# Performance work log

Hardware: AMD Instinct MI355X
Metric: run time of the kernel (lower is better)

## Reference

```python
import jax, jax.numpy as jnp
import numpy as np

BINS = 73
VMIN = -10.0
VMAX = 10.0
EPS = 1e-5


def _bn_conv(x, g, b):
    # x: [B, C, N], batch-norm (training mode) over (batch, spatial)
    m = x.mean(axis=(0, 2), keepdims=True)
    v = x.var(axis=(0, 2), keepdims=True)
    return (x - m) * jax.lax.rsqrt(v + EPS) * g[None, :, None] + b[None, :, None]


def _bn_fc(x, g, b):
    # x: [B, C]
    m = x.mean(axis=0, keepdims=True)
    v = x.var(axis=0, keepdims=True)
    return (x - m) * jax.lax.rsqrt(v + EPS) * g[None, :] + b[None, :]


def _batch_hist(x):
    # Faithful port of the torch offset-trick histc + argmax pooling.
    # x: [B, F, N] -> [B, F] float (argmax bin index per (batch, feature))
    B, F, N = x.shape
    span = VMAX - VMIN  # 20.0
    # linspace(0, span*F*B, F*B+1)[:-1] has step exactly span
    offsets = span * jnp.arange(B * F, dtype=x.dtype)  # [B*F]
    xf = x.reshape(B * F, N) + offsets[:, None]
    total_bins = BINS * B * F
    total_max = span * B * F + VMIN
    width = (total_max - VMIN) / total_bins  # == span / BINS
    flat = xf.reshape(-1)
    idx = jnp.floor((flat - VMIN) / width).astype(jnp.int32)
    # torch.histc ignores out-of-range values; values == max fall in last bin
    in_range = (flat >= VMIN) & (flat <= total_max)
    idx = jnp.clip(idx, 0, total_bins - 1)
    counts = jnp.zeros(total_bins, dtype=x.dtype).at[idx].add(
        in_range.astype(x.dtype))
    hist = counts.reshape(B, F, BINS)
    # torch.max returns first max index, as does jnp.argmax
    return jnp.argmax(hist, axis=2).astype(x.dtype)  # [B, F]


def _forward(x, w1, b1, g1, be1, w2, b2, g2, be2, w3, b3, g3, be3,
             fw1, fb1, g4, be4, fw2, fb2, g5, be5, fw3, fb3):
    B = x.shape[0]
    # pointwise conv (k=1) == channel matmul
    h = jax.nn.relu(_bn_conv(jnp.einsum('oc,bcn->bon', w1, x) + b1[None, :, None], g1, be1))
    h = jax.nn.relu(_bn_conv(jnp.einsum('oc,bcn->bon', w2, h) + b2[None, :, None], g2, be2))
    h = jax.nn.relu(_bn_conv(jnp.einsum('oc,bcn->bon', w3, h) + b3[None, :, None], g3, be3))
    feat = jax.lax.stop_gradient(_batch_hist(h))  # [B, 1024]; hist/argmax is non-differentiable in torch too
    h = jax.nn.relu(_bn_fc(feat @ fw1.T + fb1, g4, be4))
    h = jax.nn.relu(_bn_fc(h @ fw2.T + fb2, g5, be5))
    out = h @ fw3.T + fb3  # [B, 9]
    iden = jnp.eye(3, dtype=x.dtype).reshape(1, 9)
    return (out + iden).reshape(-1, 3, 3)


def setup_inputs() -> dict:
    key = jax.random.key(0)
    ks = jax.random.split(key, 12)
    B, N = 16, 2048

    def w(k, shape):
        fan_in = shape[-1]
        return (jax.random.normal(k, shape) / np.sqrt(fan_in)).astype(jnp.float32)

    f32 = jnp.float32
    return {
        'x': jax.random.normal(ks[0], (B, 3, N), dtype=f32),
        'w1': w(ks[1], (64, 3)), 'b1': jnp.zeros(64, f32),
        'g1': jnp.ones(64, f32), 'be1': jnp.zeros(64, f32),
        'w2': w(ks[2], (128, 64)), 'b2': jnp.zeros(128, f32),
        'g2': jnp.ones(128, f32), 'be2': jnp.zeros(128, f32),
        'w3': w(ks[3], (1024, 128)), 'b3': jnp.zeros(1024, f32),
        'g3': jnp.ones(1024, f32), 'be3': jnp.zeros(1024, f32),
        'fw1': w(ks[4], (512, 1024)), 'fb1': jnp.zeros(512, f32),
        'g4': jnp.ones(512, f32), 'be4': jnp.zeros(512, f32),
        'fw2': w(ks[5], (256, 512)), 'fb2': jnp.zeros(256, f32),
        'g5': jnp.ones(256, f32), 'be5': jnp.zeros(256, f32),
        'fw3': w(ks[6], (9, 256)), 'fb3': jnp.zeros(9, f32),
    }


def reference(x, w1, b1, g1, be1, w2, b2, g2, be2, w3, b3, g3, be3,
              fw1, fb1, g4, be4, fw2, fb2, g5, be5, fw3, fb3):
    return _forward(x, w1, b1, g1, be1, w2, b2, g2, be2, w3, b3, g3, be3,
                    fw1, fb1, g4, be4, fw2, fb2, g5, be5, fw3, fb3)
```

## Files before the change

kernel.cpp:

```cpp
#include <hip/hip_runtime.h>
#include <math.h>

static constexpr int Bsz  = 16;
static constexpr int Npts = 2048;
static constexpr int C1 = 64, C2 = 128, C3 = 1024;
static constexpr int NBINS = 73;
static constexpr int NROWS = Bsz * C3;
static constexpr int TOTAL = NBINS * NROWS;
static constexpr float VMINf = -10.0f;
static constexpr float TOTAL_MAXf = 327670.0f;

__device__ __forceinline__ float bnrelu(float x, float m, float inv, float g, float be) {
    float t = ((x - m) * inv) * g + be;
    return t > 0.0f ? t : 0.0f;
}

__global__ __launch_bounds__(256)
void conv1_kernel(const float* __restrict__ x, const float* __restrict__ w,
                  const float* __restrict__ bias, float* __restrict__ out) {
    __shared__ float ws[C1 * 3];
    __shared__ float bs[C1];
    int tid = threadIdx.x;
    if (tid < C1 * 3) ws[tid] = w[tid];
    if (tid < C1) bs[tid] = bias[tid];
    __syncthreads();
    int p = blockIdx.x * 256 + tid;
    int b = p >> 9;
    int nq = p & 511;
    const float* xb = x + (size_t)b * 3 * Npts;
    float4 x0 = ((const float4*)xb)[nq];
    float4 x1 = ((const float4*)(xb + Npts))[nq];
    float4 x2 = ((const float4*)(xb + 2 * Npts))[nq];
    float* o = out + (size_t)b * C1 * Npts + nq * 4;
    #pragma unroll
    for (int c = 0; c < C1; ++c) {
        float w0 = ws[c * 3], w1 = ws[c * 3 + 1], w2 = ws[c * 3 + 2], bv = bs[c];
        float4 r;
        r.x = fmaf(w0, x0.x, fmaf(w1, x1.x, fmaf(w2, x2.x, bv)));
        r.y = fmaf(w0, x0.y, fmaf(w1, x1.y, fmaf(w2, x2.y, bv)));
        r.z = fmaf(w0, x0.z, fmaf(w1, x1.z, fmaf(w2, x2.z, bv)));
        r.w = fmaf(w0, x0.w, fmaf(w1, x1.w, fmaf(w2, x2.w, bv)));
        *(float4*)(o + (size_t)c * Npts) = r;
    }
}

__global__ __launch_bounds__(256)
void stats_partial_kernel(const float* __restrict__ in,
                          double* __restrict__ sum, double* __restrict__ sumsq) {
    int c = blockIdx.x >> 2;
    int qb = blockIdx.x & 3;
    int tid = threadIdx.x;
    double s = 0.0, q = 0.0;
    for (int bb = qb * 4; bb < qb * 4 + 4; ++bb) {
        const float4* p = (const float4*)(in + ((size_t)bb * C1 + c) * Npts);
        for (int n = tid; n < Npts / 4; n += 256) {
            float4 v = p[n];
            double a0 = v.x, a1 = v.y, a2 = v.z, a3 = v.w;
            s += a0 + a1 + a2 + a3;
            q += a0 * a0 + a1 * a1 + a2 * a2 + a3 * a3;
        }
    }
    __shared__ double sh_s[256];
    __shared__ double sh_q[256];
    sh_s[tid] = s; sh_q[tid] = q;
    __syncthreads();
    for (int off = 128; off > 0; off >>= 1) {
        if (tid < off) { sh_s[tid] += sh_s[tid + off]; sh_q[tid] += sh_q[tid + off]; }
        __syncthreads();
    }
    if (tid == 0) {
        unsafeAtomicAdd(&sum[c], sh_s[0]);
        unsafeAtomicAdd(&sumsq[c], sh_q[0]);
    }
}

__global__ __launch_bounds__(256)
void finalize_stats_kernel(const double* __restrict__ s, const double* __restrict__ q, int C,
                           float* __restrict__ mout, float* __restrict__ iout) {
    int c = blockIdx.x * 256 + threadIdx.x;
    if (c >= C) return;
    double cnt = (double)Bsz * (double)Npts;
    double m = s[c] / cnt;
    double var = q[c] / cnt - m * m;
    mout[c] = (float)m;
    iout[c] = (float)(1.0 / sqrt(var + 1e-5));
}

template<int CIN, int COUT>
__global__ __launch_bounds__(256, 4)
void conv_bn_128(const float* __restrict__ in, const float* __restrict__ W,
                 const float* __restrict__ bias,
                 const float* __restrict__ m, const float* __restrict__ inv,
                 const float* __restrict__ g, const float* __restrict__ be,
                 float* __restrict__ out,
                 double* __restrict__ sum, double* __restrict__ sumsq) {
    constexpr int KT = 16;
    __shared__ float Ws[KT][128];
    __shared__ float Xs[KT][128];
    const int tid = threadIdx.x;
    const int nBase = blockIdx.x * 128;
    const int oBase = blockIdx.y * 128;
    const int b = blockIdx.z;
    const int ty = tid >> 4, tx = tid & 15;
    const int w_o = tid >> 1, w_k0 = (tid & 1) * 8;
    const int x_c = tid >> 4;
    const int x_nA = (tid & 15) * 4;
    float acc[8][8] = {};

    for (int kBase = 0; kBase < CIN; kBase += KT) {
        const float* wp = W + (size_t)(oBase + w_o) * CIN + kBase + w_k0;
        float4 wa = *(const float4*)wp;
        float4 wb = *(const float4*)(wp + 4);
        int c = kBase + x_c;
        float mm = m[c], ii = inv[c], gg = g[c], bb = be[c];
        const float* xp = in + ((size_t)b * CIN + c) * Npts + nBase;
        float4 xa = *(const float4*)(xp + x_nA);
        float4 xb2 = *(const float4*)(xp + 64 + x_nA);

        Ws[w_k0 + 0][w_o] = wa.x; Ws[w_k0 + 1][w_o] = wa.y;
        Ws[w_k0 + 2][w_o] = wa.z; Ws[w_k0 + 3][w_o] = wa.w;
        Ws[w_k0 + 4][w_o] = wb.x; Ws[w_k0 + 5][w_o] = wb.y;
        Ws[w_k0 + 6][w_o] = wb.z; Ws[w_k0 + 7][w_o] = wb.w;

        float4 s0, s1;
        s0.x = bnrelu(xa.x, mm, ii, gg, bb); s0.y = bnrelu(xa.y, mm, ii, gg, bb);
        s0.z = bnrelu(xa.z, mm, ii, gg, bb); s0.w = bnrelu(xa.w, mm, ii, gg, bb);
        s1.x = bnrelu(xb2.x, mm, ii, gg, bb); s1.y = bnrelu(xb2.y, mm, ii, gg, bb);
        s1.z = bnrelu(xb2.z, mm, ii, gg, bb); s1.w = bnrelu(xb2.w, mm, ii, gg, bb);
        *(float4*)&Xs[x_c][x_nA] = s0;
        *(float4*)&Xs[x_c][64 + x_nA] = s1;

        __syncthreads();
        #pragma unroll
        for (int kk = 0; kk < KT; ++kk) {
            float4 wA = *(const float4*)&Ws[kk][ty * 8];
            float4 wB = *(const float4*)&Ws[kk][ty * 8 + 4];
            float4 xA = *(const float4*)&Xs[kk][tx * 4];
            float4 xB = *(const float4*)&Xs[kk][64 + tx * 4];
            float wr[8] = {wA.x, wA.y, wA.z, wA.w, wB.x, wB.y, wB.z, wB.w};
            float xr[8] = {xA.x, xA.y, xA.z, xA.w, xB.x, xB.y, xB.z, xB.w};
            #pragma unroll
            for (int i = 0; i < 8; ++i)
                #pragma unroll
                for (int j = 0; j < 8; ++j)
                    acc[i][j] = fmaf(wr[i], xr[j], acc[i][j]);
        }
        __syncthreads();
    }

    #pragma unroll
    for (int i = 0; i < 8; ++i) {
        int o = oBase + ty * 8 + i;
        float bv = bias[o];
        float v[8];
        #pragma unroll
        for (int j = 0; j < 8; ++j) v[j] = acc[i][j] + bv;
        float* op = out + ((size_t)b * COUT + o) * Npts + nBase;
        *(float4*)(op + tx * 4)      = make_float4(v[0], v[1], v[2], v[3]);
        *(float4*)(op + 64 + tx * 4) = make_float4(v[4], v[5], v[6], v[7]);
        double si = 0.0, qi = 0.0;
        #pragma unroll
        for (int j = 0; j < 8; ++j) { double dv = (double)v[j]; si += dv; qi += dv * dv; }
        #pragma unroll
        for (int off = 1; off < 16; off <<= 1) {
            si += __shfl_xor(si, off, 64);
            qi += __shfl_xor(qi, off, 64);
        }
        if (tx == 0) {
            unsafeAtomicAdd(&sum[o], si);
            unsafeAtomicAdd(&sumsq[o], qi);
        }
    }
}

template<int CIN, int COUT>
__global__ __launch_bounds__(256)
void conv_bn_64(const float* __restrict__ in, const float* __restrict__ W,
                const float* __restrict__ bias,
                const float* __restrict__ m, const float* __restrict__ inv,
                const float* __restrict__ g, const float* __restrict__ be,
                float* __restrict__ out,
                double* __restrict__ sum, double* __restrict__ sumsq) {
    constexpr int KT = 32;
    __shared__ float Ws[KT][64];
    __shared__ float Xs[KT][64];
    int tid = threadIdx.x;
    int nBase = blockIdx.x * 64;
    int oBase = blockIdx.y * 64;
    int b = blockIdx.z;
    int ty = tid / 16, tx = tid % 16;
    float acc[4][4] = {};

    int w_o  = tid / 4;
    int w_k0 = (tid % 4) * 8;
    int x_c  = tid / 8;
    int x_n0 = (tid % 8) * 8;

    for (int kBase = 0; kBase < CIN; kBase += KT) {
        const float* wp = W + (size_t)(oBase + w_o) * CIN + kBase + w_k0;
        float4 wa = *(const float4*)wp;
        float4 wb = *(const float4*)(wp + 4);
        float wv[8] = {wa.x, wa.y, wa.z, wa.w, wb.x, wb.y, wb.z, wb.w};
        #pragma unroll
        for (int i = 0; i < 8; ++i) Ws[w_k0 + i][w_o] = wv[i];

        int c = kBase + x_c;
        float mm = m[c], ii = inv[c], gg = g[c], bb = be[c];
        const float* xp = in + ((size_t)b * CIN + c) * Npts + nBase + x_n0;
        float4 xa = *(const float4*)xp;
        float4 xb = *(const float4*)(xp + 4);
        float xv[8] = {xa.x, xa.y, xa.z, xa.w, xb.x, xb.y, xb.z, xb.w};
        #pragma unroll
        for (int i = 0; i < 8; ++i) Xs[x_c][x_n0 + i] = bnrelu(xv[i], mm, ii, gg, bb);

        __syncthreads();
        #pragma unroll
        for (int kk = 0; kk < KT; ++kk) {
            float4 w4 = *(const float4*)(&Ws[kk][ty * 4]);
            float4 x4 = *(const float4*)(&Xs[kk][tx * 4]);
            float wr[4] = {w4.x, w4.y, w4.z, w4.w};
            float xr[4] = {x4.x, x4.y, x4.z, x4.w};
            #pragma unroll
            for (int i = 0; i < 4; ++i)
                #pragma unroll
                for (int j = 0; j < 4; ++j)
                    acc[i][j] = fmaf(wr[i], xr[j], acc[i][j]);
        }
        __syncthreads();
    }

    #pragma unroll
    for (int i = 0; i < 4; ++i) {
        int o = oBase + ty * 4 + i;
        float bv = bias[o];
        float v[4] = {acc[i][0] + bv, acc[i][1] + bv, acc[i][2] + bv, acc[i][3] + bv};
        *(float4*)(out + ((size_t)b * COUT + o) * Npts + nBase + tx * 4) =
            make_float4(v[0], v[1], v[2], v[3]);
        double si = 0.0, qi = 0.0;
        #pragma unroll
        for (int j = 0; j < 4; ++j) { double dv = (double)v[j]; si += dv; qi += dv * dv; }
        #pragma unroll
        for (int off = 1; off < 16; off <<= 1) {
            si += __shfl_xor(si, off, 64);
            qi += __shfl_xor(qi, off, 64);
        }
        if (tx == 0) {
            unsafeAtomicAdd(&sum[o], si);
            unsafeAtomicAdd(&sumsq[o], qi);
        }
    }
}

__global__ __launch_bounds__(256)
void hist_kernel(const float* __restrict__ h3,
                 const float* __restrict__ m, const float* __restrict__ inv,
                 const float* __restrict__ g, const float* __restrict__ be,
                 unsigned* __restrict__ counts) {
    __shared__ unsigned bins[4][80];
    int row = blockIdx.x;
    int f = row & (C3 - 1);
    int tid = threadIdx.x;
    int wv = tid >> 6;
    for (int i = tid; i < 4 * 80; i += 256) ((unsigned*)bins)[i] = 0u;
    __syncthreads();
    float mm = m[f], ii = inv[f], gg = g[f], bb = be[f];
    float off = 20.0f * (float)row;
    const float4* p4 = (const float4*)(h3 + (size_t)row * Npts);
    const float WIDTH = (float)(327680.0 / 1196032.0);
    int rbase = row * NBINS;
    int zc = 0;
    for (int n = tid; n < Npts / 4; n += 256) {
        float4 xv = p4[n];
        float vv[4] = {xv.x, xv.y, xv.z, xv.w};
        #pragma unroll
        for (int j = 0; j < 4; ++j) {
            float v = bnrelu(vv[j], mm, ii, gg, bb);
            if (v == 0.0f) { ++zc; continue; }
            float flat = v + off;
            if (flat >= VMINf && flat <= TOTAL_MAXf) {
                int idx = (int)floorf((flat - VMINf) / WIDTH);
                if (idx > TOTAL - 1) idx = TOTAL - 1;
                if (idx < 0) idx = 0;
                int local = idx - rbase;
                if (local >= 0 && local < NBINS) atomicAdd(&bins[wv][local], 1u);
                else atomicAdd(&counts[idx], 1u);
            }
        }
    }
    #pragma unroll
    for (int o = 32; o >= 1; o >>= 1) zc += __shfl_xor(zc, o, 64);
    if ((tid & 63) == 0 && zc) atomicAdd(&bins[wv][36], (unsigned)zc);
    __syncthreads();
    if (tid < NBINS) {
        unsigned t = bins[0][tid] + bins[1][tid] + bins[2][tid] + bins[3][tid];
        if (t) atomicAdd(&counts[rbase + tid], t);
    }
}

__global__ __launch_bounds__(256)
void argmax_kernel(const unsigned* __restrict__ counts, float* __restrict__ feat) {
    int row = blockIdx.x * 256 + threadIdx.x;
    if (row >= NROWS) return;
    const unsigned* c = counts + (size_t)row * NBINS;
    unsigned best = c[0]; int bi = 0;
    #pragma unroll 8
    for (int i = 1; i < NBINS; ++i) {
        unsigned v = c[i];
        if (v > best) { best = v; bi = i; }
    }
    feat[row] = (float)bi;
}

template<int K, int COUT>
__global__ __launch_bounds__(256)
void fc_bn_relu_kernel(const float* __restrict__ in, const float* __restrict__ W,
                       const float* __restrict__ bias,
                       const float* __restrict__ g, const float* __restrict__ be,
                       float* __restrict__ out) {
    int j = blockIdx.x;
    int tid = threadIdx.x;
    int b = tid / 16;
    int l = tid % 16;
    const float* wrow = W + (size_t)j * K;
    const float* xrow = in + (size_t)b * K;
    float s = 0.0f;
    for (int k = l; k < K; k += 16) s = fmaf(xrow[k], wrow[k], s);
    #pragma unroll
    for (int o = 8; o >= 1; o >>= 1) s += __shfl_xor(s, o, 64);
    __shared__ float vals[Bsz];
    __shared__ float stat[2];
    if (l == 0) vals[b] = s + bias[j];
    __syncthreads();
    if (tid == 0) {
        double a = 0.0, q = 0.0;
        for (int i = 0; i < Bsz; ++i) { double v = vals[i]; a += v; q += v * v; }
        double mm = a / Bsz;
        double var = q / Bsz - mm * mm;
        stat[0] = (float)mm;
        stat[1] = (float)(1.0 / sqrt(var + 1e-5));
    }
    __syncthreads();
    if (tid < Bsz) {
        float t = ((vals[tid] - stat[0]) * stat[1]) * g[j] + be[j];
        out[(size_t)tid * COUT + j] = t > 0.0f ? t : 0.0f;
    }
}

__global__ __launch_bounds__(256)
void fc3_kernel(const float* __restrict__ in, const float* __restrict__ W,
                const float* __restrict__ bias, float* __restrict__ out) {
    int t = threadIdx.x;
    if (t >= Bsz * 9) return;
    int b = t / 9, j = t % 9;
    const float* x = in + (size_t)b * 256;
    const float* w = W + (size_t)j * 256;
    float s = 0.0f;
    for (int k = 0; k < 256; ++k) s = fmaf(x[k], w[k], s);
    s += bias[j];
    if (j == 0 || j == 4 || j == 8) s += 1.0f;
    out[t] = s;
}

extern "C" void kernel_launch(void* const* d_in, const int* in_sizes, int n_in,
                              void* d_out, int out_size, void* d_ws, size_t ws_size,
                              hipStream_t stream) {
    const float* x   = (const float*)d_in[0];
    const float* w1  = (const float*)d_in[1];
    const float* b1  = (const float*)d_in[2];
    const float* g1  = (const float*)d_in[3];
    const float* be1 = (const float*)d_in[4];
    const float* w2  = (const float*)d_in[5];
    const float* b2  = (const float*)d_in[6];
    const float* g2  = (const float*)d_in[7];
    const float* be2 = (const float*)d_in[8];
    const float* w3  = (const float*)d_in[9];
    const float* b3  = (const float*)d_in[10];
    const float* g3  = (const float*)d_in[11];
    const float* be3 = (const float*)d_in[12];
    const float* fw1 = (const float*)d_in[13];
    const float* fb1 = (const float*)d_in[14];
    const float* g4  = (const float*)d_in[15];
    const float* be4 = (const float*)d_in[16];
    const float* fw2 = (const float*)d_in[17];
    const float* fb2 = (const float*)d_in[18];
    const float* g5  = (const float*)d_in[19];
    const float* be5 = (const float*)d_in[20];
    const float* fw3 = (const float*)d_in[21];
    const float* fb3 = (const float*)d_in[22];

    double* sum1 = (double*)d_ws;
    double* q1d  = sum1 + C1;
    double* sum2 = q1d + C1;
    double* q2   = sum2 + C2;
    double* sum3 = q2 + C2;
    double* q3   = sum3 + C3;
    unsigned* counts = (unsigned*)(q3 + C3);
    float* h1 = (float*)(counts + TOTAL);
    float* h2 = h1 + (size_t)Bsz * C1 * Npts;
    float* h3 = h2 + (size_t)Bsz * C2 * Npts;
    float* m1 = h3 + (size_t)Bsz * C3 * Npts;
    float* i1 = m1 + C1;
    float* m2 = i1 + C1;
    float* i2 = m2 + C2;
    float* m3 = i2 + C2;
    float* i3 = m3 + C3;
    float* feat = i3 + C3;
    float* h4 = feat + NROWS;
    float* h5 = h4 + Bsz * 512;

    size_t zero_bytes = (size_t)(2 * C1 + 2 * C2 + 2 * C3) * sizeof(double)
                      + (size_t)TOTAL * sizeof(unsigned);
    hipMemsetAsync(d_ws, 0, zero_bytes, stream);

    conv1_kernel<<<dim3(Bsz * Npts / 4 / 256), 256, 0, stream>>>(x, w1, b1, h1);
    stats_partial_kernel<<<dim3(C1 * 4), 256, 0, stream>>>(h1, sum1, q1d);
    finalize_stats_kernel<<<dim3(1), 256, 0, stream>>>(sum1, q1d, C1, m1, i1);
    conv_bn_64<C1, C2><<<dim3(Npts / 64, C2 / 64, Bsz), 256, 0, stream>>>(
        h1, w2, b2, m1, i1, g1, be1, h2, sum2, q2);
    finalize_stats_kernel<<<dim3(1), 256, 0, stream>>>(sum2, q2, C2, m2, i2);
    conv_bn_128<C2, C3><<<dim3(Npts / 128, C3 / 128, Bsz), 256, 0, stream>>>(
        h2, w3, b3, m2, i2, g2, be2, h3, sum3, q3);
    finalize_stats_kernel<<<dim3(C3 / 256), 256, 0, stream>>>(sum3, q3, C3, m3, i3);
    hist_kernel<<<dim3(NROWS), 256, 0, stream>>>(h3, m3, i3, g3, be3, counts);
    argmax_kernel<<<dim3(NROWS / 256), 256, 0, stream>>>(counts, feat);
    fc_bn_relu_kernel<1024, 512><<<dim3(512), 256, 0, stream>>>(feat, fw1, fb1, g4, be4, h4);
    fc_bn_relu_kernel<512, 256><<<dim3(256), 256, 0, stream>>>(h4, fw2, fb2, g5, be5, h5);
    fc3_kernel<<<dim3(1), 256, 0, stream>>>(h5, fw3, fb3, (float*)d_out);
}
```

Measured before the change: 361.5 us.

## Run conv3 on bf16 MFMA with transposed activations and bf16 h3 storage

Replaces the fp32 SIMT 128->1024 pointwise conv with a bf16 MFMA kernel. A new transpose kernel applies BN+ReLU to h2 and writes it point-major in bf16. The conv output h3 is stored as bf16, which halves the traffic into the histogram kernel. The risk is that bf16 rounding of activations, weights and h3 moves values across histogram bin edges and changes argmax results relative to the fp32 reference.

```diff
diff --git a/kernel.cpp b/kernel.cpp
--- a/kernel.cpp
+++ b/kernel.cpp
@@ -10,9 +10,17 @@
 static constexpr float VMINf = -10.0f;
 static constexpr float TOTAL_MAXf = 327670.0f;
 
+typedef __attribute__((ext_vector_type(8))) short short8v;
+typedef __attribute__((ext_vector_type(4))) float f32x4;
+
 __device__ __forceinline__ float bnrelu(float x, float m, float inv, float g, float be) {
     float t = ((x - m) * inv) * g + be;
     return t > 0.0f ? t : 0.0f;
+}
+
+__device__ __forceinline__ ushort f2bf(float f) {
+    uint u = __float_as_uint(f);
+    return (ushort)((u + 0x7FFFu + ((u >> 16) & 1u)) >> 16);
 }
 
 __global__ __launch_bounds__(256)
@@ -84,93 +92,6 @@
     double var = q[c] / cnt - m * m;
     mout[c] = (float)m;
     iout[c] = (float)(1.0 / sqrt(var + 1e-5));
-}
-
-template<int CIN, int COUT>
-__global__ __launch_bounds__(256, 4)
-void conv_bn_128(const float* __restrict__ in, const float* __restrict__ W,
-                 const float* __restrict__ bias,
-                 const float* __restrict__ m, const float* __restrict__ inv,
-                 const float* __restrict__ g, const float* __restrict__ be,
-                 float* __restrict__ out,
-                 double* __restrict__ sum, double* __restrict__ sumsq) {
-    constexpr int KT = 16;
-    __shared__ float Ws[KT][128];
-    __shared__ float Xs[KT][128];
-    const int tid = threadIdx.x;
-    const int nBase = blockIdx.x * 128;
-    const int oBase = blockIdx.y * 128;
-    const int b = blockIdx.z;
-    const int ty = tid >> 4, tx = tid & 15;
-    const int w_o = tid >> 1, w_k0 = (tid & 1) * 8;
-    const int x_c = tid >> 4;
-    const int x_nA = (tid & 15) * 4;
-    float acc[8][8] = {};
-
-    for (int kBase = 0; kBase < CIN; kBase += KT) {
-        const float* wp = W + (size_t)(oBase + w_o) * CIN + kBase + w_k0;
-        float4 wa = *(const float4*)wp;
-        float4 wb = *(const float4*)(wp + 4);
-        int c = kBase + x_c;
-        float mm = m[c], ii = inv[c], gg = g[c], bb = be[c];
-        const float* xp = in + ((size_t)b * CIN + c) * Npts + nBase;
-        float4 xa = *(const float4*)(xp + x_nA);
-        float4 xb2 = *(const float4*)(xp + 64 + x_nA);
-
-        Ws[w_k0 + 0][w_o] = wa.x; Ws[w_k0 + 1][w_o] = wa.y;
-        Ws[w_k0 + 2][w_o] = wa.z; Ws[w_k0 + 3][w_o] = wa.w;
-        Ws[w_k0 + 4][w_o] = wb.x; Ws[w_k0 + 5][w_o] = wb.y;
-        Ws[w_k0 + 6][w_o] = wb.z; Ws[w_k0 + 7][w_o] = wb.w;
-
-        float4 s0, s1;
-        s0.x = bnrelu(xa.x, mm, ii, gg, bb); s0.y = bnrelu(xa.y, mm, ii, gg, bb);
-        s0.z = bnrelu(xa.z, mm, ii, gg, bb); s0.w = bnrelu(xa.w, mm, ii, gg, bb);
-        s1.x = bnrelu(xb2.x, mm, ii, gg, bb); s1.y = bnrelu(xb2.y, mm, ii, gg, bb);
-        s1.z = bnrelu(xb2.z, mm, ii, gg, bb); s1.w = bnrelu(xb2.w, mm, ii, gg, bb);
-        *(float4*)&Xs[x_c][x_nA] = s0;
-        *(float4*)&Xs[x_c][64 + x_nA] = s1;
-
-        __syncthreads();
-        #pragma unroll
-        for (int kk = 0; kk < KT; ++kk) {
-            float4 wA = *(const float4*)&Ws[kk][ty * 8];
-            float4 wB = *(const float4*)&Ws[kk][ty * 8 + 4];
-            float4 xA = *(const float4*)&Xs[kk][tx * 4];
-            float4 xB = *(const float4*)&Xs[kk][64 + tx * 4];
-            float wr[8] = {wA.x, wA.y, wA.z, wA.w, wB.x, wB.y, wB.z, wB.w};
-            float xr[8] = {xA.x, xA.y, xA.z, xA.w, xB.x, xB.y, xB.z, xB.w};
-            #pragma unroll
-            for (int i = 0; i < 8; ++i)
-                #pragma unroll
-                for (int j = 0; j < 8; ++j)
-                    acc[i][j] = fmaf(wr[i], xr[j], acc[i][j]);
-        }
-        __syncthreads();
-    }
-
-    #pragma unroll
-    for (int i = 0; i < 8; ++i) {
-        int o = oBase + ty * 8 + i;
-        float bv = bias[o];
-        float v[8];
-        #pragma unroll
-        for (int j = 0; j < 8; ++j) v[j] = acc[i][j] + bv;
-        float* op = out + ((size_t)b * COUT + o) * Npts + nBase;
-        *(float4*)(op + tx * 4)      = make_float4(v[0], v[1], v[2], v[3]);
-        *(float4*)(op + 64 + tx * 4) = make_float4(v[4], v[5], v[6], v[7]);
-        double si = 0.0, qi = 0.0;
-        #pragma unroll
-        for (int j = 0; j < 8; ++j) { double dv = (double)v[j]; si += dv; qi += dv * dv; }
-        #pragma unroll
-        for (int off = 1; off < 16; off <<= 1) {
-            si += __shfl_xor(si, off, 64);
-            qi += __shfl_xor(qi, off, 64);
-        }
-        if (tx == 0) {
-            unsafeAtomicAdd(&sum[o], si);
-            unsafeAtomicAdd(&sumsq[o], qi);
-        }
-    }
 }
 
 template<int CIN, int COUT>
@@ -252,7 +173,123 @@
 }
 
 __global__ __launch_bounds__(256)
-void hist_kernel(const float* __restrict__ h3,
+void transpose_bnrelu_kernel(const float* __restrict__ in,
+                             const float* __restrict__ m, const float* __restrict__ inv,
+                             const float* __restrict__ g, const float* __restrict__ be,
+                             ushort* __restrict__ out) {
+    __shared__ ushort Ls[C2 * 72];
+    __shared__ float pm[C2], pi[C2], pg[C2], pb[C2];
+    int tid = threadIdx.x;
+    int n0 = blockIdx.x * 64;
+    int b = blockIdx.y;
+    if (tid < C2) { pm[tid] = m[tid]; pi[tid] = inv[tid]; pg[tid] = g[tid]; pb[tid] = be[tid]; }
+    __syncthreads();
+    #pragma unroll
+    for (int it = 0; it < 8; ++it) {
+        int q = it * 256 + tid;
+        int c = q >> 4, nq = q & 15;
+        float4 v = *(const float4*)(in + ((size_t)b * C2 + c) * Npts + n0 + nq * 4);
+        float mm = pm[c], ii = pi[c], gg = pg[c], bb = pb[c];
+        uint lo = (uint)f2bf(bnrelu(v.x, mm, ii, gg, bb)) |
+                  ((uint)f2bf(bnrelu(v.y, mm, ii, gg, bb)) << 16);
+        uint hi = (uint)f2bf(bnrelu(v.z, mm, ii, gg, bb)) |
+                  ((uint)f2bf(bnrelu(v.w, mm, ii, gg, bb)) << 16);
+        *(uint2*)(&Ls[c * 72 + nq * 4]) = make_uint2(lo, hi);
+    }
+    __syncthreads();
+    int n = tid >> 2, cs = (tid & 3) * 32;
+    uint w[16];
+    #pragma unroll
+    for (int j = 0; j < 16; ++j) {
+        w[j] = (uint)Ls[(cs + 2 * j) * 72 + n] | ((uint)Ls[(cs + 2 * j + 1) * 72 + n] << 16);
+    }
+    ushort* op = out + ((size_t)b * Npts + n0 + n) * C2 + cs;
+    *(uint4*)(op)      = make_uint4(w[0],  w[1],  w[2],  w[3]);
+    *(uint4*)(op + 8)  = make_uint4(w[4],  w[5],  w[6],  w[7]);
+    *(uint4*)(op + 16) = make_uint4(w[8],  w[9],  w[10], w[11]);
+    *(uint4*)(op + 24) = make_uint4(w[12], w[13], w[14], w[15]);
+}
+
+__global__ __launch_bounds__(256)
+void conv3_mfma_kernel(const ushort* __restrict__ xt, const float* __restrict__ W,
+                       const float* __restrict__ bias, ushort* __restrict__ out,
+                       double* __restrict__ sum, double* __restrict__ sumsq) {
+    constexpr int LDW = 136;
+    __shared__ ushort Wl[64 * LDW];
+    __shared__ ushort Xl[128 * LDW];
+    const int tid = threadIdx.x;
+    const int nBase = blockIdx.x * 128;
+    const int oBase = blockIdx.y * 64;
+    const int b = blockIdx.z;
+
+    #pragma unroll
+    for (int it = 0; it < 8; ++it) {
+        int q = it * 256 + tid;
+        int r = q >> 5, cq = q & 31;
+        float4 v = *(const float4*)(W + (size_t)(oBase + r) * C2 + cq * 4);
+        uint lo = (uint)f2bf(v.x) | ((uint)f2bf(v.y) << 16);
+        uint hi = (uint)f2bf(v.z) | ((uint)f2bf(v.w) << 16);
+        *(uint2*)(&Wl[r * LDW + cq * 4]) = make_uint2(lo, hi);
+    }
+    const ushort* xb = xt + ((size_t)b * Npts + nBase) * C2;
+    #pragma unroll
+    for (int it = 0; it < 8; ++it) {
+        int o8 = it * 256 + tid;
+        int r = o8 >> 4, c8 = o8 & 15;
+        uint4 v = *(const uint4*)(xb + (size_t)r * C2 + c8 * 8);
+        *(uint4*)(&Xl[r * LDW + c8 * 8]) = v;
+    }
+    __syncthreads();
+
+    const int wv = tid >> 6, lane = tid & 63, lr = lane & 15, lg = lane >> 4;
+    f32x4 acc[4][2];
+    #pragma unroll
+    for (int i = 0; i < 4; ++i) {
+        #pragma unroll
+        for (int j = 0; j < 2; ++j) { f32x4 z = {0.f, 0.f, 0.f, 0.f}; acc[i][j] = z; }
+    }
+
+    #pragma unroll
+    for (int ks = 0; ks < 4; ++ks) {
+        const int ko = ks * 32 + lg * 8;
+        short8v b0 = *(const short8v*)(&Xl[(wv * 32 + lr) * LDW + ko]);
+        short8v b1 = *(const short8v*)(&Xl[(wv * 32 + 16 + lr) * LDW + ko]);
+        #pragma unroll
+        for (int fo = 0; fo < 4; ++fo) {
+            short8v a = *(const short8v*)(&Wl[(fo * 16 + lr) * LDW + ko]);
+            acc[fo][0] = __builtin_amdgcn_mfma_f32_16x16x32_bf16(a, b0, acc[fo][0], 0, 0, 0);
+            acc[fo][1] = __builtin_amdgcn_mfma_f32_16x16x32_bf16(a, b1, acc[fo][1], 0, 0, 0);
+        }
+    }
+
+    #pragma unroll
+    for (int fo = 0; fo < 4; ++fo) {
+        #pragma unroll
+        for (int rg = 0; rg < 4; ++rg) {
+            int o = oBase + fo * 16 + lg * 4 + rg;
+            float bv = bias[o];
+            float v0 = acc[fo][0][rg] + bv;
+            float v1 = acc[fo][1][rg] + bv;
+            size_t rowoff = ((size_t)b * C3 + o) * Npts + nBase + wv * 32;
+            out[rowoff + lr]      = f2bf(v0);
+            out[rowoff + 16 + lr] = f2bf(v1);
+            double s  = (double)v0 + (double)v1;
+            double qq = (double)v0 * v0 + (double)v1 * v1;
+            #pragma unroll
+            for (int off = 1; off < 16; off <<= 1) {
+                s  += __shfl_xor(s,  off, 64);
+                qq += __shfl_xor(qq, off, 64);
+            }
+            if (lr == 0) {
+                unsafeAtomicAdd(&sum[o],   s);
+                unsafeAtomicAdd(&sumsq[o], qq);
+            }
+        }
+    }
+}
+
+__global__ __launch_bounds__(256)
+void hist_kernel(const ushort* __restrict__ h3,
                  const float* __restrict__ m, const float* __restrict__ inv,
                  const float* __restrict__ g, const float* __restrict__ be,
                  unsigned* __restrict__ counts) {
@@ -265,16 +302,20 @@
     __syncthreads();
     float mm = m[f], ii = inv[f], gg = g[f], bb = be[f];
     float off = 20.0f * (float)row;
-    const float4* p4 = (const float4*)(h3 + (size_t)row * Npts);
+    const uint4* p4 = (const uint4*)(h3 + (size_t)row * Npts);
     const float WIDTH = (float)(327680.0 / 1196032.0);
     int rbase = row * NBINS;
     int zc = 0;
-    for (int n = tid; n < Npts / 4; n += 256) {
-        float4 xv = p4[n];
-        float vv[4] = {xv.x, xv.y, xv.z, xv.w};
-        #pragma unroll
-        for (int j = 0; j < 4; ++j) {
-            float v = bnrelu(vv[j], mm, ii, gg, bb);
+    uint4 q = p4[tid];
+    uint wsv[4] = {q.x, q.y, q.z, q.w};
+    #pragma unroll
+    for (int j = 0; j < 4; ++j) {
+        float vlo = __uint_as_float(wsv[j] << 16);
+        float vhi = __uint_as_float(wsv[j] & 0xFFFF0000u);
+        float pair[2] = {vlo, vhi};
+        #pragma unroll
+        for (int h = 0; h < 2; ++h) {
+            float v = bnrelu(pair[h], mm, ii, gg, bb);
             if (v == 0.0f) { ++zc; continue; }
             float flat = v + off;
             if (flat >= VMINf && flat <= TOTAL_MAXf) {
@@ -397,8 +438,7 @@
     unsigned* counts = (unsigned*)(q3 + C3);
     float* h1 = (float*)(counts + TOTAL);
     float* h2 = h1 + (size_t)Bsz * C1 * Npts;
-    float* h3 = h2 + (size_t)Bsz * C2 * Npts;
-    float* m1 = h3 + (size_t)Bsz * C3 * Npts;
+    float* m1 = h2 + (size_t)Bsz * C2 * Npts;
     float* i1 = m1 + C1;
     float* m2 = i1 + C1;
     float* i2 = m2 + C2;
@@ -407,6 +447,8 @@
     float* feat = i3 + C3;
     float* h4 = feat + NROWS;
     float* h5 = h4 + Bsz * 512;
+    ushort* h2t = (ushort*)(h5 + Bsz * 256);
+    ushort* h3  = h2t + (size_t)Bsz * Npts * C2;
 
     size_t zero_bytes = (size_t)(2 * C1 + 2 * C2 + 2 * C3) * sizeof(double)
                       + (size_t)TOTAL * sizeof(unsigned);
@@ -418,8 +460,10 @@
     conv_bn_64<C1, C2><<<dim3(Npts / 64, C2 / 64, Bsz), 256, 0, stream>>>(
         h1, w2, b2, m1, i1, g1, be1, h2, sum2, q2);
     finalize_stats_kernel<<<dim3(1), 256, 0, stream>>>(sum2, q2, C2, m2, i2);
-    conv_bn_128<C2, C3><<<dim3(Npts / 128, C3 / 128, Bsz), 256, 0, stream>>>(
-        h2, w3, b3, m2, i2, g2, be2, h3, sum3, q3);
+    transpose_bnrelu_kernel<<<dim3(Npts / 64, Bsz), 256, 0, stream>>>(
+        h2, m2, i2, g2, be2, h2t);
+    conv3_mfma_kernel<<<dim3(Npts / 128, C3 / 64, Bsz), 256, 0, stream>>>(
+        h2t, w3, b3, h3, sum3, q3);
     finalize_stats_kernel<<<dim3(C3 / 256), 256, 0, stream>>>(sum3, q3, C3, m3, i3);
     hist_kernel<<<dim3(NROWS), 256, 0, stream>>>(h3, m3, i3, g3, be3, counts);
     argmax_kernel<<<dim3(NROWS / 256), 256, 0, stream>>>(counts, feat);
```

Result: slower. 401.5 us (+11.1%).
